# Kernel tuning notes

Hardware: AMD Instinct MI355X
Metric: run time of the kernel (lower is better)

Reference implementation:

```python
import jax, jax.numpy as jnp
import numpy as np

B, N, C = 16, 1024, 256
NH, DH = 8, 32          # dense attention heads
NHD, P = 8, 4           # deformable heads / sampling points
Hs = Ws = 32            # value spatial grid (N == Hs*Ws)
HID = 1024              # mlp hidden = 4*C


def setup_inputs() -> dict:
    key = jax.random.key(0)
    ks = jax.random.split(key, 16)
    rn = lambda i, shape, s=1.0: jax.random.normal(ks[i], shape, jnp.float32) * s
    return {
        "x": rn(0, (B, N, C)),
        "ref": jax.random.uniform(ks[1], (B, N, 2), jnp.float32),
        "value": rn(2, (B, N, C)),
        "ln1_w": jnp.ones((C,), jnp.float32), "ln1_b": jnp.zeros((C,), jnp.float32),
        "ln2_w": jnp.ones((C,), jnp.float32), "ln2_b": jnp.zeros((C,), jnp.float32),
        "ln3_w": jnp.ones((C,), jnp.float32), "ln3_b": jnp.zeros((C,), jnp.float32),
        "qkv_w": rn(3, (3 * C, C), 0.05),
        "proj_w": rn(4, (C, C), 0.05), "proj_b": jnp.zeros((C,), jnp.float32),
        "off_w": rn(5, (NHD * P * 2, C), 0.01), "off_b": rn(6, (NHD * P * 2,), 0.5),
        "aw_w": rn(7, (NHD * P, C), 0.01), "aw_b": jnp.zeros((NHD * P,), jnp.float32),
        "vproj_w": rn(8, (C, C), 0.05), "vproj_b": jnp.zeros((C,), jnp.float32),
        "oproj_w": rn(9, (C, C), 0.05), "oproj_b": jnp.zeros((C,), jnp.float32),
        "fc1_w": rn(10, (HID, C), 0.05), "fc1_b": jnp.zeros((HID,), jnp.float32),
        "fc2_w": rn(11, (C, HID), 0.05), "fc2_b": jnp.zeros((C,), jnp.float32),
    }


def _ln(x, w, b):
    m = x.mean(-1, keepdims=True)
    v = ((x - m) ** 2).mean(-1, keepdims=True)
    return (x - m) * jax.lax.rsqrt(v + 1e-5) * w + b


def _attn(x, qkv_w, proj_w, proj_b):
    qkv = (x @ qkv_w.T).reshape(B, N, 3, NH, DH)
    q, k, v = qkv[:, :, 0], qkv[:, :, 1], qkv[:, :, 2]
    a = jnp.einsum('bqhd,bkhd->bhqk', q, k) * (DH ** -0.5)
    a = jax.nn.softmax(a, axis=-1)
    o = jnp.einsum('bhqk,bkhd->bqhd', a, v).reshape(B, N, C)
    return o @ proj_w.T + proj_b


def _deform(q, ref, value, off_w, off_b, aw_w, aw_b, vproj_w, vproj_b, oproj_w, oproj_b):
    # single-level MS deformable attention (Deformable-DETR style)
    v = (value @ vproj_w.T + vproj_b).reshape(B, Hs * Ws, NHD, DH)
    off = (q @ off_w.T + off_b).reshape(B, N, NHD, P, 2)
    aw = jax.nn.softmax((q @ aw_w.T + aw_b).reshape(B, N, NHD, P), axis=-1)
    norm = jnp.array([Ws, Hs], jnp.float32)
    loc = ref[:, :, None, None, :] + off / norm  # [B,N,NHD,P,2] normalized coords
    gx = loc[..., 0] * Ws - 0.5
    gy = loc[..., 1] * Hs - 0.5
    x0 = jnp.floor(gx); y0 = jnp.floor(gy)
    lx = gx - x0; ly = gy - y0
    x0i = x0.astype(jnp.int32); y0i = y0.astype(jnp.int32)
    b_idx = jnp.arange(B)[:, None, None, None]
    h_idx = jnp.arange(NHD)[None, None, :, None]

    def gather(xi, yi):
        valid = ((xi >= 0) & (xi < Ws) & (yi >= 0) & (yi < Hs)).astype(jnp.float32)
        idx = jnp.clip(yi, 0, Hs - 1) * Ws + jnp.clip(xi, 0, Ws - 1)
        return v[b_idx, idx, h_idx] * valid[..., None]  # [B,N,NHD,P,DH]

    s = (gather(x0i, y0i) * ((1 - lx) * (1 - ly))[..., None]
         + gather(x0i + 1, y0i) * (lx * (1 - ly))[..., None]
         + gather(x0i, y0i + 1) * ((1 - lx) * ly)[..., None]
         + gather(x0i + 1, y0i + 1) * (lx * ly)[..., None])
    out = (s * aw[..., None]).sum(axis=3).reshape(B, N, C)
    return out @ oproj_w.T + oproj_b


def reference(x, ref, value, ln1_w, ln1_b, ln2_w, ln2_b, ln3_w, ln3_b,
              qkv_w, proj_w, proj_b, off_w, off_b, aw_w, aw_b,
              vproj_w, vproj_b, oproj_w, oproj_b, fc1_w, fc1_b, fc2_w, fc2_b):
    x = x + _attn(_ln(x, ln1_w, ln1_b), qkv_w, proj_w, proj_b)
    x = x + _deform(_ln(x, ln2_w, ln2_b), ref, value,
                    off_w, off_b, aw_w, aw_b, vproj_w, vproj_b, oproj_w, oproj_b)
    h = jax.nn.gelu(_ln(x, ln3_w, ln3_b) @ fc1_w.T + fc1_b, approximate=False) @ fc2_w.T + fc2_b
    return x + h
```

## Files before the change

### kernel.cpp

```cpp
#include <hip/hip_runtime.h>
#include <hip/hip_bf16.h>

#define Bq   16
#define Nq   1024
#define Cq   256
#define NHq  8
#define DHq  32
#define HIDq 1024
#define BNq  (Bq * Nq)

typedef float f32x4 __attribute__((ext_vector_type(4)));
typedef short bf16x8 __attribute__((ext_vector_type(8)));
typedef unsigned short ushort_t;

__device__ __forceinline__ unsigned int f2bf(float f) {
    unsigned int u = __builtin_bit_cast(unsigned int, f);
    u = (u + 0x7fffu + ((u >> 16) & 1u)) >> 16;
    return u & 0xffffu;
}
__device__ __forceinline__ unsigned int packbf2(float a, float b) {
    unsigned int ua = __builtin_bit_cast(unsigned int, a) + 0x8000u;
    unsigned int ub = __builtin_bit_cast(unsigned int, b) + 0x8000u;
    return __builtin_amdgcn_perm(ub, ua, 0x07060302);
}
__device__ __forceinline__ float gelu_t(float x) {
    float y = x * (0.7978845608028654f + 0.035677408136300125f * x * x);
    float e = __builtin_amdgcn_exp2f(y * 2.8853900817779268f);
    return x - x / (1.f + e);
}

typedef __attribute__((address_space(1))) const unsigned int* gas_u32;
typedef __attribute__((address_space(3))) unsigned int* las_u32;
__device__ __forceinline__ void gload16(const void* g, void* l) {
    __builtin_amdgcn_global_load_lds((gas_u32)g, (las_u32)l, 16, 0, 0);
}

struct CastSeg { const float* src; ushort_t* dst; int nblk; int n; };
struct CastArgs { CastSeg s[9]; };

__global__ __launch_bounds__(256) void castm(CastArgs a) {
    int bid = blockIdx.x;
    int seg = 0, acc = 0;
    for (seg = 0; seg < 9; seg++) {
        if (bid < acc + a.s[seg].nblk) break;
        acc += a.s[seg].nblk;
    }
    const CastSeg sg = a.s[seg];
    int i = (bid - acc) * 1024 + threadIdx.x * 4;
    if (i < sg.n) {
        float4 v = *(const float4*)(sg.src + i);
        uint2 u;
        u.x = packbf2(v.x, v.y);
        u.y = packbf2(v.z, v.w);
        *(uint2*)(sg.dst + i) = u;
    }
}

__global__ __launch_bounds__(256) void ln_kernel(const float* __restrict__ X,
                                                 const float* __restrict__ w,
                                                 const float* __restrict__ b,
                                                 ushort_t* __restrict__ Y) {
    int wave = threadIdx.x >> 6, lane = threadIdx.x & 63;
    int t = blockIdx.x * 4 + wave;
    float4 v = *(const float4*)(X + (size_t)t * Cq + lane * 4);
    float s = v.x + v.y + v.z + v.w;
#pragma unroll
    for (int d = 1; d < 64; d <<= 1) s += __shfl_xor(s, d);
    float mean = s * (1.f / 256.f);
    float4 dv = {v.x - mean, v.y - mean, v.z - mean, v.w - mean};
    float q = dv.x * dv.x + dv.y * dv.y + dv.z * dv.z + dv.w * dv.w;
#pragma unroll
    for (int d = 1; d < 64; d <<= 1) q += __shfl_xor(q, d);
    float rs = rsqrtf(q * (1.f / 256.f) + 1e-5f);
    float4 wv = *(const float4*)(w + lane * 4);
    float4 bv = *(const float4*)(b + lane * 4);
    uint2 u;
    u.x = packbf2(dv.x * rs * wv.x + bv.x, dv.y * rs * wv.y + bv.y);
    u.y = packbf2(dv.z * rs * wv.z + bv.z, dv.w * rs * wv.w + bv.w);
    *(uint2*)(Y + (size_t)t * Cq + lane * 4) = u;
}

template <int OMODE, bool GELU_, bool RESID, int KT>
__global__ __launch_bounds__(256) void mgemm(const ushort_t* __restrict__ A,
                                             const ushort_t* __restrict__ W,
                                             const float* __restrict__ bias,
                                             const float* __restrict__ R,
                                             void* __restrict__ OutP,
                                             int M, int Nn) {
    __shared__ __align__(16) ushort_t Al[4096];
    __shared__ __align__(16) ushort_t Bl[4096];
    int m0 = blockIdx.x * 128, n0 = blockIdx.y * 128;
    int tid = threadIdx.x;
    int w = tid >> 6, lane = tid & 63;
    int l15 = lane & 15, quad = lane >> 4;
    int wrow = w >> 1, wcol = w & 1;

    f32x4 acc[4][4];
#pragma unroll
    for (int i = 0; i < 4; i++)
#pragma unroll
        for (int j = 0; j < 4; j++) acc[i][j] = (f32x4){0.f, 0.f, 0.f, 0.f};

    const ushort_t* gA0 = A + (size_t)(m0 + lane) * KT + w * 8;
    const ushort_t* gA1 = A + (size_t)(m0 + 64 + lane) * KT + w * 8;
    const ushort_t* gB0 = W + (size_t)(n0 + lane) * KT + w * 8;
    const ushort_t* gB1 = W + (size_t)(n0 + 64 + lane) * KT + w * 8;
    ushort_t* lA0 = &Al[(w * 128) * 8];
    ushort_t* lA1 = &Al[(w * 128 + 64) * 8];
    ushort_t* lB0 = &Bl[(w * 128) * 8];
    ushort_t* lB1 = &Bl[(w * 128 + 64) * 8];

#pragma unroll
    for (int k0 = 0; k0 < KT; k0 += 32) {
        gload16(gA0 + k0, lA0);
        gload16(gA1 + k0, lA1);
        gload16(gB0 + k0, lB0);
        gload16(gB1 + k0, lB1);
        __syncthreads();

        bf16x8 aF[4], bF[4];
#pragma unroll
        for (int i = 0; i < 4; i++)
            aF[i] = *(const bf16x8*)&Al[(quad * 128 + wrow * 64 + i * 16 + l15) * 8];
#pragma unroll
        for (int j = 0; j < 4; j++)
            bF[j] = *(const bf16x8*)&Bl[(quad * 128 + wcol * 64 + j * 16 + l15) * 8];
#pragma unroll
        for (int i = 0; i < 4; i++)
#pragma unroll
            for (int j = 0; j < 4; j++)
                acc[i][j] = __builtin_amdgcn_mfma_f32_16x16x32_bf16(bF[j], aF[i], acc[i][j], 0, 0, 0);
        __syncthreads();
    }

#pragma unroll
    for (int i = 0; i < 4; i++) {
        int mg = m0 + wrow * 64 + i * 16 + l15;
#pragma unroll
        for (int j = 0; j < 4; j++) {
            int ng = n0 + wcol * 64 + j * 16 + quad * 4;
            if (ng >= Nn) continue;
            f32x4 rv = acc[i][j];
            if constexpr (OMODE == 1) {
                int which = ng >> 8;
                int h = (ng >> 5) & 7;
                int d = ng & 31;
                int bb = mg >> 10, nn = mg & 1023;
                ushort_t* qb = (ushort_t*)OutP;
                if (which == 2) {
                    size_t dst = 2 * (size_t)BNq * Cq +
                                 ((size_t)(bb * 8 + h) * 32 + d) * 1024 + nn;
#pragma unroll
                    for (int r = 0; r < 4; r++)
                        qb[dst + (size_t)r * 1024] = (ushort_t)f2bf(rv[r]);
                } else {
                    if (which == 0) {
                        const float sc = 0.17677669529663687f * 1.4426950408889634f;
                        rv[0] *= sc; rv[1] *= sc; rv[2] *= sc; rv[3] *= sc;
                    }
                    size_t dst = (size_t)which * ((size_t)BNq * Cq) +
                                 ((size_t)(bb * 8 + h) * 1024 + nn) * 32 + d;
                    uint2 pk;
                    pk.x = packbf2(rv[0], rv[1]);
                    pk.y = packbf2(rv[2], rv[3]);
                    *(uint2*)(qb + dst) = pk;
                }
            } else {
                if (bias) {
                    float4 bv = *(const float4*)(bias + ng);
                    rv[0] += bv.x; rv[1] += bv.y; rv[2] += bv.z; rv[3] += bv.w;
                }
                if (GELU_) {
#pragma unroll
                    for (int r = 0; r < 4; r++) rv[r] = gelu_t(rv[r]);
                }
                if constexpr (OMODE == 2) {
                    uint2 pk;
                    pk.x = packbf2(rv[0], rv[1]);
                    pk.y = packbf2(rv[2], rv[3]);
                    *(uint2*)((ushort_t*)OutP + (size_t)mg * Nn + ng) = pk;
                } else {
                    if (RESID) {
                        float4 rr = *(const float4*)(R + (size_t)mg * Nn + ng);
                        rv[0] += rr.x; rv[1] += rr.y; rv[2] += rr.z; rv[3] += rr.w;
                    }
                    *(float4*)((float*)OutP + (size_t)mg * Nn + ng) =
                        make_float4(rv[0], rv[1], rv[2], rv[3]);
                }
            }
        }
    }
}

__global__ __launch_bounds__(256) void attn_mfma(const ushort_t* __restrict__ Qb,
                                                 const ushort_t* __restrict__ Kb,
                                                 const ushort_t* __restrict__ Vtg,
                                                 ushort_t* __restrict__ o) {
    int bh = blockIdx.x;
    int b = bh >> 3, h = bh & 7;
    int q0 = blockIdx.y * 128;
    int tid = threadIdx.x;
    int wave = tid >> 6, lane = tid & 63;
    int l15 = lane & 15, quad = lane >> 4;

    __shared__ __align__(16) ushort_t Ps[4][32][72];

    const size_t hb = (size_t)bh * 32768;

    bf16x8 qfrag[2];
#pragma unroll
    for (int g = 0; g < 2; g++)
        qfrag[g] = *(const bf16x8*)(Qb + hb + (size_t)(q0 + wave * 32 + g * 16 + l15) * 32 + quad * 8);

    const ushort_t* kfp = Kb + hb + (size_t)l15 * 32 + quad * 8;
    const ushort_t* vfp0 = Vtg + hb + (size_t)l15 * 1024 + quad * 8;
    const ushort_t* vfp1 = Vtg + hb + (size_t)(l15 + 16) * 1024 + quad * 8;

    bf16x8 ones;
#pragma unroll
    for (int i = 0; i < 8; i++) ones[i] = (short)0x3F80;

    f32x4 oa[2][2];
#pragma unroll
    for (int g = 0; g < 2; g++)
#pragma unroll
        for (int t = 0; t < 2; t++) oa[g][t] = (f32x4){0.f, 0.f, 0.f, 0.f};
    f32x4 osum[2] = {(f32x4){0.f, 0.f, 0.f, 0.f}, (f32x4){0.f, 0.f, 0.f, 0.f}};

    bf16x8 kf[4];
#pragma unroll
    for (int kg = 0; kg < 4; kg++)
        kf[kg] = *(const bf16x8*)(kfp + (size_t)(kg * 16) * 32);

    for (int kt = 0; kt < 16; kt++) {
        bf16x8 kfn[4];
        if (kt < 15) {
#pragma unroll
            for (int kg = 0; kg < 4; kg++)
                kfn[kg] = *(const bf16x8*)(kfp + (size_t)((kt + 1) * 64 + kg * 16) * 32);
        }
        const f32x4 z = {0.f, 0.f, 0.f, 0.f};
#pragma unroll
        for (int g = 0; g < 2; g++) {
#pragma unroll
            for (int kg = 0; kg < 4; kg++) {
                f32x4 st = __builtin_amdgcn_mfma_f32_16x16x32_bf16(kf[kg], qfrag[g], z, 0, 0, 0);
                float e0 = __builtin_amdgcn_exp2f(st[0]);
                float e1 = __builtin_amdgcn_exp2f(st[1]);
                float e2 = __builtin_amdgcn_exp2f(st[2]);
                float e3 = __builtin_amdgcn_exp2f(st[3]);
                uint2 pk;
                pk.x = packbf2(e0, e1);
                pk.y = packbf2(e2, e3);
                *(uint2*)&Ps[wave][g * 16 + l15][kg * 16 + quad * 4] = pk;
            }
        }
#pragma unroll
        for (int c = 0; c < 2; c++) {
            bf16x8 vb0 = *(const bf16x8*)(vfp0 + kt * 64 + c * 32);
            bf16x8 vb1 = *(const bf16x8*)(vfp1 + kt * 64 + c * 32);
#pragma unroll
            for (int g = 0; g < 2; g++) {
                bf16x8 pa = *(const bf16x8*)&Ps[wave][g * 16 + l15][c * 32 + quad * 8];
                oa[g][0] = __builtin_amdgcn_mfma_f32_16x16x32_bf16(pa, vb0, oa[g][0], 0, 0, 0);
                oa[g][1] = __builtin_amdgcn_mfma_f32_16x16x32_bf16(pa, vb1, oa[g][1], 0, 0, 0);
                osum[g] = __builtin_amdgcn_mfma_f32_16x16x32_bf16(pa, ones, osum[g], 0, 0, 0);
            }
        }
#pragma unroll
        for (int kg = 0; kg < 4; kg++) kf[kg] = kfn[kg];
    }

#pragma unroll
    for (int g = 0; g < 2; g++) {
#pragma unroll
        for (int r = 0; r < 4; r++) {
            float inv = 1.f / osum[g][r];
            int q = q0 + wave * 32 + g * 16 + quad * 4 + r;
            ushort_t* orow = o + ((size_t)(b * 1024 + q)) * 256 + h * 32;
            orow[l15] = (ushort_t)f2bf(oa[g][0][r] * inv);
            orow[l15 + 16] = (ushort_t)f2bf(oa[g][1][r] * inv);
        }
    }
}

__global__ __launch_bounds__(256) void deform_kernel(const float* __restrict__ ref,
                                                     const float* __restrict__ off,
                                                     const float* __restrict__ awl,
                                                     const float* __restrict__ v,
                                                     ushort_t* __restrict__ out) {
    int t = blockIdx.x;
    int b = t >> 10;
    int tid = threadIdx.x;
    int h = tid >> 5, d = tid & 31;

    float rx = ref[(size_t)t * 2 + 0];
    float ry = ref[(size_t)t * 2 + 1];
    const float* offr = off + (size_t)t * 64 + h * 8;
    const float* awr = awl + (size_t)t * 32 + h * 4;

    float L0 = awr[0], L1 = awr[1], L2 = awr[2], L3 = awr[3];
    float mm = fmaxf(fmaxf(L0, L1), fmaxf(L2, L3));
    float e0 = __expf(L0 - mm), e1 = __expf(L1 - mm), e2 = __expf(L2 - mm), e3 = __expf(L3 - mm);
    float inv = 1.f / (e0 + e1 + e2 + e3);
    float aw[4] = {e0 * inv, e1 * inv, e2 * inv, e3 * inv};

    const float* vb = v + (size_t)b * Nq * Cq + h * 32 + d;

    float s = 0.f;
#pragma unroll
    for (int p = 0; p < 4; p++) {
        float gx = rx * 32.f + offr[p * 2 + 0] - 0.5f;
        float gy = ry * 32.f + offr[p * 2 + 1] - 0.5f;
        float x0f = floorf(gx), y0f = floorf(gy);
        float lx = gx - x0f, ly = gy - y0f;
        int x0 = (int)x0f, y0 = (int)y0f;
        auto g = [&](int xi, int yi) -> float {
            if (xi < 0 || xi > 31 || yi < 0 || yi > 31) return 0.f;
            return vb[(size_t)(yi * 32 + xi) * Cq];
        };
        float sp = g(x0, y0) * (1.f - lx) * (1.f - ly)
                 + g(x0 + 1, y0) * lx * (1.f - ly)
                 + g(x0, y0 + 1) * (1.f - lx) * ly
                 + g(x0 + 1, y0 + 1) * lx * ly;
        s += aw[p] * sp;
    }
    out[(size_t)t * Cq + h * 32 + d] = (ushort_t)f2bf(s);
}

extern "C" void kernel_launch(void* const* d_in, const int* in_sizes, int n_in,
                              void* d_out, int out_size, void* d_ws, size_t ws_size,
                              hipStream_t stream) {
    const size_t S = (size_t)BNq * Cq;
    float* ws = (float*)d_ws;
    float* X = ws;
    ushort_t* Ybf = (ushort_t*)(ws + S);
    ushort_t* Wbf = (ushort_t*)(ws + S + S / 2);

    ushort_t* Wqkv   = Wbf;
    ushort_t* Wproj  = Wbf + 196608;
    ushort_t* Woff   = Wbf + 262144;
    ushort_t* Waw    = Wbf + 278528;
    ushort_t* Wvproj = Wbf + 286720;
    ushort_t* Woproj = Wbf + 352256;
    ushort_t* Wfc1   = Wbf + 417792;
    ushort_t* Wfc2   = Wbf + 679936;

    ushort_t* QKVbf = (ushort_t*)(ws + 2 * S);
    ushort_t* O1bf  = (ushort_t*)(ws + 2 * S + 3 * S / 2);
    float* Vb   = ws + 2 * S + S / 2;
    float* OffB = ws + 2 * S + 3 * S / 2;
    float* AwB  = OffB + (size_t)BNq * 64;
    ushort_t* Sbbf = (ushort_t*)(AwB + (size_t)BNq * 32);
    ushort_t* Hbbf = (ushort_t*)(ws + 2 * S);
    ushort_t* Valbf = (ushort_t*)(ws + 9 * S / 2);

    auto fp = [&](int i) { return (const float*)d_in[i]; };
    const float* x_in = fp(0);

    CastArgs ca;
    ca.s[0] = {fp(9),  Wqkv,   192, 196608};
    ca.s[1] = {fp(10), Wproj,  64,  65536};
    ca.s[2] = {fp(12), Woff,   16,  16384};
    ca.s[3] = {fp(14), Waw,    8,   8192};
    ca.s[4] = {fp(16), Wvproj, 64,  65536};
    ca.s[5] = {fp(18), Woproj, 64,  65536};
    ca.s[6] = {fp(20), Wfc1,   256, 262144};
    ca.s[7] = {fp(22), Wfc2,   256, 262144};
    ca.s[8] = {fp(2),  Valbf,  4096, (int)S};
    castm<<<5016, 256, 0, stream>>>(ca);

    ln_kernel<<<BNq / 4, 256, 0, stream>>>(x_in, fp(3), fp(4), Ybf);
    mgemm<1, false, false, 256><<<dim3(128, 6), 256, 0, stream>>>(
        Ybf, Wqkv, nullptr, nullptr, QKVbf, BNq, 768);
    attn_mfma<<<dim3(128, 8), 256, 0, stream>>>(
        QKVbf, QKVbf + S, QKVbf + 2 * S, O1bf);
    mgemm<0, false, true, 256><<<dim3(128, 2), 256, 0, stream>>>(
        O1bf, Wproj, fp(11), x_in, X, BNq, 256);

    ln_kernel<<<BNq / 4, 256, 0, stream>>>(X, fp(5), fp(6), Ybf);
    mgemm<0, false, false, 256><<<dim3(128, 2), 256, 0, stream>>>(
        Valbf, Wvproj, fp(17), nullptr, Vb, BNq, 256);
    mgemm<0, false, false, 256><<<dim3(128, 1), 256, 0, stream>>>(
        Ybf, Woff, fp(13), nullptr, OffB, BNq, 64);
    mgemm<0, false, false, 256><<<dim3(128, 1), 256, 0, stream>>>(
        Ybf, Waw, fp(15), nullptr, AwB, BNq, 32);
    deform_kernel<<<BNq, 256, 0, stream>>>(fp(1), OffB, AwB, Vb, Sbbf);
    mgemm<0, false, true, 256><<<dim3(128, 2), 256, 0, stream>>>(
        Sbbf, Woproj, fp(19), X, X, BNq, 256);

    ln_kernel<<<BNq / 4, 256, 0, stream>>>(X, fp(7), fp(8), Ybf);
    mgemm<2, true, false, 256><<<dim3(128, 8), 256, 0, stream>>>(
        Ybf, Wfc1, fp(21), nullptr, Hbbf, BNq, 1024);
    mgemm<0, false, true, 1024><<<dim3(128, 2), 256, 0, stream>>>(
        Hbbf, Wfc2, fp(23), X, d_out, BNq, 256);
}
```

Before: 375.1 us.

## Feed softmax probabilities to PV MFMA directly from registers, drop LDS staging

The attention kernel now takes the exponentiated score fragment produced by the QK^T MFMA and uses it as the B operand of 16x16x16 bf16 MFMAs for the PV product and the row-sum, so the per-wave LDS round-trip through Ps is removed. V fragments are loaded as 4-element vectors and prefetched one tile ahead alongside K. The output layout becomes transposed (queries along lanes), so the epilogue writes packed 4-element bf16 stores per row. In exchange it issues twice as many smaller MFMAs (16x16x16 instead of 16x16x32), holds more registers for the V prefetch, and uses narrower global V loads.

```diff
diff --git a/kernel.cpp b/kernel.cpp
--- a/kernel.cpp
+++ b/kernel.cpp
@@ -11,6 +11,7 @@
 
 typedef float f32x4 __attribute__((ext_vector_type(4)));
 typedef short bf16x8 __attribute__((ext_vector_type(8)));
+typedef short bf16x4 __attribute__((ext_vector_type(4)));
 typedef unsigned short ushort_t;
 
 __device__ __forceinline__ unsigned int f2bf(float f) {
@@ -203,8 +204,6 @@
     int wave = tid >> 6, lane = tid & 63;
     int l15 = lane & 15, quad = lane >> 4;
 
-    __shared__ __align__(16) ushort_t Ps[4][32][72];
-
     const size_t hb = (size_t)bh * 32768;
 
     bf16x8 qfrag[2];
@@ -213,12 +212,12 @@
         qfrag[g] = *(const bf16x8*)(Qb + hb + (size_t)(q0 + wave * 32 + g * 16 + l15) * 32 + quad * 8);
 
     const ushort_t* kfp = Kb + hb + (size_t)l15 * 32 + quad * 8;
-    const ushort_t* vfp0 = Vtg + hb + (size_t)l15 * 1024 + quad * 8;
-    const ushort_t* vfp1 = Vtg + hb + (size_t)(l15 + 16) * 1024 + quad * 8;
-
-    bf16x8 ones;
-#pragma unroll
-    for (int i = 0; i < 8; i++) ones[i] = (short)0x3F80;
+    const ushort_t* vfp0 = Vtg + hb + (size_t)l15 * 1024 + quad * 4;
+    const ushort_t* vfp1 = Vtg + hb + (size_t)(l15 + 16) * 1024 + quad * 4;
+
+    bf16x4 onesA;
+#pragma unroll
+    for (int i = 0; i < 4; i++) onesA[i] = (short)0x3F80;
 
     f32x4 oa[2][2];
 #pragma unroll
@@ -228,22 +227,30 @@
     f32x4 osum[2] = {(f32x4){0.f, 0.f, 0.f, 0.f}, (f32x4){0.f, 0.f, 0.f, 0.f}};
 
     bf16x8 kf[4];
-#pragma unroll
-    for (int kg = 0; kg < 4; kg++)
+    bf16x4 vf[4][2];
+#pragma unroll
+    for (int kg = 0; kg < 4; kg++) {
         kf[kg] = *(const bf16x8*)(kfp + (size_t)(kg * 16) * 32);
+        vf[kg][0] = *(const bf16x4*)(vfp0 + kg * 16);
+        vf[kg][1] = *(const bf16x4*)(vfp1 + kg * 16);
+    }
 
     for (int kt = 0; kt < 16; kt++) {
         bf16x8 kfn[4];
+        bf16x4 vfn[4][2];
         if (kt < 15) {
 #pragma unroll
-            for (int kg = 0; kg < 4; kg++)
+            for (int kg = 0; kg < 4; kg++) {
                 kfn[kg] = *(const bf16x8*)(kfp + (size_t)((kt + 1) * 64 + kg * 16) * 32);
+                vfn[kg][0] = *(const bf16x4*)(vfp0 + (kt + 1) * 64 + kg * 16);
+                vfn[kg][1] = *(const bf16x4*)(vfp1 + (kt + 1) * 64 + kg * 16);
+            }
         }
         const f32x4 z = {0.f, 0.f, 0.f, 0.f};
 #pragma unroll
-        for (int g = 0; g < 2; g++) {
-#pragma unroll
-            for (int kg = 0; kg < 4; kg++) {
+        for (int kg = 0; kg < 4; kg++) {
+#pragma unroll
+            for (int g = 0; g < 2; g++) {
                 f32x4 st = __builtin_amdgcn_mfma_f32_16x16x32_bf16(kf[kg], qfrag[g], z, 0, 0, 0);
                 float e0 = __builtin_amdgcn_exp2f(st[0]);
                 float e1 = __builtin_amdgcn_exp2f(st[1]);
@@ -252,35 +259,32 @@
                 uint2 pk;
                 pk.x = packbf2(e0, e1);
                 pk.y = packbf2(e2, e3);
-                *(uint2*)&Ps[wave][g * 16 + l15][kg * 16 + quad * 4] = pk;
+                bf16x4 pB = __builtin_bit_cast(bf16x4, pk);
+                oa[g][0] = __builtin_amdgcn_mfma_f32_16x16x16bf16_1k(vf[kg][0], pB, oa[g][0], 0, 0, 0);
+                oa[g][1] = __builtin_amdgcn_mfma_f32_16x16x16bf16_1k(vf[kg][1], pB, oa[g][1], 0, 0, 0);
+                osum[g]  = __builtin_amdgcn_mfma_f32_16x16x16bf16_1k(onesA, pB, osum[g], 0, 0, 0);
             }
         }
 #pragma unroll
-        for (int c = 0; c < 2; c++) {
-            bf16x8 vb0 = *(const bf16x8*)(vfp0 + kt * 64 + c * 32);
-            bf16x8 vb1 = *(const bf16x8*)(vfp1 + kt * 64 + c * 32);
-#pragma unroll
-            for (int g = 0; g < 2; g++) {
-                bf16x8 pa = *(const bf16x8*)&Ps[wave][g * 16 + l15][c * 32 + quad * 8];
-                oa[g][0] = __builtin_amdgcn_mfma_f32_16x16x32_bf16(pa, vb0, oa[g][0], 0, 0, 0);
-                oa[g][1] = __builtin_amdgcn_mfma_f32_16x16x32_bf16(pa, vb1, oa[g][1], 0, 0, 0);
-                osum[g] = __builtin_amdgcn_mfma_f32_16x16x32_bf16(pa, ones, osum[g], 0, 0, 0);
-            }
+        for (int kg = 0; kg < 4; kg++) {
+            kf[kg] = kfn[kg];
+            vf[kg][0] = vfn[kg][0];
+            vf[kg][1] = vfn[kg][1];
         }
-#pragma unroll
-        for (int kg = 0; kg < 4; kg++) kf[kg] = kfn[kg];
     }
 
 #pragma unroll
     for (int g = 0; g < 2; g++) {
-#pragma unroll
-        for (int r = 0; r < 4; r++) {
-            float inv = 1.f / osum[g][r];
-            int q = q0 + wave * 32 + g * 16 + quad * 4 + r;
-            ushort_t* orow = o + ((size_t)(b * 1024 + q)) * 256 + h * 32;
-            orow[l15] = (ushort_t)f2bf(oa[g][0][r] * inv);
-            orow[l15 + 16] = (ushort_t)f2bf(oa[g][1][r] * inv);
-        }
+        float inv = 1.f / osum[g][0];
+        int q = q0 + wave * 32 + g * 16 + l15;
+        ushort_t* orow = o + ((size_t)(b * 1024 + q)) * 256 + h * 32;
+        uint2 p0, p1;
+        p0.x = packbf2(oa[g][0][0] * inv, oa[g][0][1] * inv);
+        p0.y = packbf2(oa[g][0][2] * inv, oa[g][0][3] * inv);
+        p1.x = packbf2(oa[g][1][0] * inv, oa[g][1][1] * inv);
+        p1.y = packbf2(oa[g][1][2] * inv, oa[g][1][3] * inv);
+        *(uint2*)(orow + quad * 4) = p0;
+        *(uint2*)(orow + 16 + quad * 4) = p1;
     }
 }
 
```

Result: slower. 413.1 us (+10.1%).
